# Optimization experiments

Measured on AMD Instinct MI355X. Metric: run time of the kernel, lower is better.

The kernel has to match this reference:

```python
import jax, jax.numpy as jnp
import numpy as np

TOP_K = 2
EPS = 1e-20


def setup_inputs() -> dict:
    key = jax.random.key(0)
    ks = jax.random.split(key, 8)
    B, S, H, E, D = 4, 2048, 1024, 8, 2048
    s = 0.02
    return {
        "x":  jax.random.normal(ks[0], (B, S, H), dtype=jnp.float32),
        "Wr": jax.random.normal(ks[1], (H, E), dtype=jnp.float32) * s,
        "Wg": jax.random.normal(ks[2], (E, H, D), dtype=jnp.float32) * s,
        "Wu": jax.random.normal(ks[3], (E, H, D), dtype=jnp.float32) * s,
        "Wd": jax.random.normal(ks[4], (E, D, H), dtype=jnp.float32) * s,
        "Sg": jax.random.normal(ks[5], (H, D), dtype=jnp.float32) * s,
        "Su": jax.random.normal(ks[6], (H, D), dtype=jnp.float32) * s,
        "Sd": jax.random.normal(ks[7], (D, H), dtype=jnp.float32) * s,
    }


def reference(x, Wr, Wg, Wu, Wd, Sg, Su, Sd):
    B, S, H = x.shape
    T = B * S
    xt = x.reshape(T, H)

    # Router: softmax scores, top-k, renormalize top-k weights
    scores = jax.nn.softmax(xt @ Wr, axis=-1)            # [T, E]
    topk_w, topk_idx = jax.lax.top_k(scores, TOP_K)      # [T, K]
    topk_w = topk_w / (topk_w.sum(axis=-1, keepdims=True) + EPS)

    # Per-expert SwiGLU FFN computed densely over all tokens (vectorized over E)
    g = jax.nn.silu(jnp.einsum('th,ehd->etd', xt, Wg))   # [E, T, D]
    u = jnp.einsum('th,ehd->etd', xt, Wu)                # [E, T, D]
    out_all = jnp.einsum('etd,edh->eth', g * u, Wd)      # [E, T, H]

    # Combine: gather each token's top-k expert outputs, weighted sum
    tok = jnp.arange(T)[:, None]                          # [T, 1]
    gathered = out_all[topk_idx, tok, :]                  # [T, K, H]
    out = jnp.sum(gathered * topk_w[..., None], axis=1).reshape(B, S, H)

    # Shared expert (applied to original input, added to MoE output)
    shared = (jax.nn.silu(x @ Sg) * (x @ Su)) @ Sd        # [B, S, H]
    return out + shared
```

## Files before the change

kernel.cpp:

```cpp
#include <hip/hip_runtime.h>
#include <stdint.h>

#define T_TOK 8192
#define HD 1024
#define ED 8
#define DD 2048
#define BM 128
#define BK 32
#define TILE_SHARED 64
#define TILE_MAX 200
#define ROWCAP 25600
#define RT_TPW 8

typedef short short8 __attribute__((ext_vector_type(8)));
typedef float f32x4 __attribute__((ext_vector_type(4)));

__device__ __forceinline__ unsigned short f2bf(float f) {
  union { float f; unsigned int u; } v; v.f = f;
  unsigned int r = (v.u + 0x7fffu + ((v.u >> 16) & 1u)) >> 16;
  return (unsigned short)r;
}

__device__ __forceinline__ void gll16(const void* g, void* l) {
  __builtin_amdgcn_global_load_lds(
      (const __attribute__((address_space(1))) unsigned int*)g,
      (__attribute__((address_space(3))) unsigned int*)l, 16, 0, 0);
}

__global__ __launch_bounds__(256) void k_zero(float* __restrict__ outp) {
  size_t i = (size_t)blockIdx.x * 256 + threadIdx.x;
  ((float4*)outp)[i] = make_float4(0.f, 0.f, 0.f, 0.f);
}

__global__ __launch_bounds__(256) void k_init(int* counts, int* tok, float* wrow) {
  int i = blockIdx.x * 256 + threadIdx.x;
  if (i < 32) counts[i] = 0;
  if (i < ROWCAP) {
    tok[i] = (i < T_TOK) ? i : 0;
    wrow[i] = (i < T_TOK) ? 1.0f : 0.0f;
  }
}

__global__ __launch_bounds__(256) void k_transpose(const float* __restrict__ in,
    unsigned short* __restrict__ outp, int R, int C) {
  __shared__ float tile[32][33];
  size_t boff = (size_t)blockIdx.z * (size_t)R * (size_t)C;
  in += boff; outp += boff;
  int c0 = blockIdx.x * 32, r0 = blockIdx.y * 32;
  int tx = threadIdx.x & 31, ty = threadIdx.x >> 5;
#pragma unroll
  for (int i = 0; i < 4; ++i)
    tile[ty + i * 8][tx] = in[(size_t)(r0 + ty + i * 8) * C + c0 + tx];
  __syncthreads();
#pragma unroll
  for (int i = 0; i < 4; ++i)
    outp[(size_t)(c0 + ty + i * 8) * R + r0 + tx] = f2bf(tile[tx][ty + i * 8]);
}

__global__ __launch_bounds__(256) void k_router(const float* __restrict__ x,
    const float* __restrict__ Wr, unsigned short* __restrict__ xb,
    int* __restrict__ counts, int* __restrict__ topE, float* __restrict__ topW) {
  __shared__ float wrT[ED * HD];
  __shared__ int hist[ED];
  int tid = threadIdx.x;
  if (tid < ED) hist[tid] = 0;
  for (int i = tid; i < ED * HD; i += 256) {
    int e = i >> 10, h = i & (HD - 1);
    wrT[i] = Wr[h * ED + e];
  }
  __syncthreads();
  int lane = tid & 63, wave = tid >> 6;
  int tbase = (blockIdx.x * 4 + wave) * RT_TPW;
  for (int tt = 0; tt < RT_TPW; ++tt) {
    int t = tbase + tt;
    const float* xrow = x + (size_t)t * HD;
    unsigned short* xbrow = xb + (size_t)t * HD;
    float acc[ED] = {0, 0, 0, 0, 0, 0, 0, 0};
#pragma unroll
    for (int i = 0; i < HD / 64; ++i) {
      int h = i * 64 + lane;
      float v = xrow[h];
      xbrow[h] = f2bf(v);
#pragma unroll
      for (int e = 0; e < ED; ++e) acc[e] += v * wrT[e * HD + h];
    }
#pragma unroll
    for (int off = 32; off; off >>= 1)
#pragma unroll
      for (int e = 0; e < ED; ++e) acc[e] += __shfl_xor(acc[e], off);
    if (lane == 0) {
      float m = acc[0];
#pragma unroll
      for (int e = 1; e < ED; ++e) m = fmaxf(m, acc[e]);
      float p[ED], s = 0.f;
#pragma unroll
      for (int e = 0; e < ED; ++e) { p[e] = __expf(acc[e] - m); s += p[e]; }
      int i0 = 0;
#pragma unroll
      for (int e = 1; e < ED; ++e) if (acc[e] > acc[i0]) i0 = e;
      int i1 = -1;
#pragma unroll
      for (int e = 0; e < ED; ++e) {
        if (e == i0) continue;
        if (i1 < 0 || acc[e] > acc[i1]) i1 = e;
      }
      float p0 = p[i0] / s, p1 = p[i1] / s;
      float rs = p0 + p1 + 1e-20f;
      topE[t * 2] = i0; topE[t * 2 + 1] = i1;
      topW[t * 2] = p0 / rs; topW[t * 2 + 1] = p1 / rs;
      atomicAdd(&hist[i0], 1);
      atomicAdd(&hist[i1], 1);
    }
  }
  __syncthreads();
  if (tid < ED) atomicAdd(&counts[tid], hist[tid]);
}

__global__ __launch_bounds__(256) void k_plan(const int* __restrict__ counts, int* cursor,
    int* __restrict__ tileE, int* __restrict__ tileEnd) {
  __shared__ int tstart[ED + 1], segend[ED];
  if (threadIdx.x == 0) {
    int base = T_TOK, rt = TILE_SHARED;
    for (int e = 0; e < ED; ++e) {
      int c = counts[e];
      cursor[e] = base;
      tstart[e] = rt;
      segend[e] = base + c;
      int tiles = (c + BM - 1) >> 7;
      rt += tiles;
      base += tiles << 7;
    }
    tstart[ED] = rt;
  }
  __syncthreads();
  for (int rt = threadIdx.x; rt < TILE_MAX; rt += 256) {
    int e = -1, end = 0;
    if (rt < TILE_SHARED) { e = ED; end = T_TOK; }
    else {
      for (int q = 0; q < ED; ++q)
        if (rt >= tstart[q] && rt < tstart[q + 1]) { e = q; end = segend[q]; }
    }
    tileE[rt] = e; tileEnd[rt] = end;
  }
}

__global__ __launch_bounds__(256) void k_scatter(const int* __restrict__ topE,
    const float* __restrict__ topW, int* cursor, int* tok, float* wrow) {
  __shared__ int lcount[ED], lbase[ED];
  int tid = threadIdx.x;
  if (tid < ED) lcount[tid] = 0;
  __syncthreads();
  int t = blockIdx.x * 256 + tid;
  int e0 = topE[t * 2], e1 = topE[t * 2 + 1];
  float w0 = topW[t * 2], w1 = topW[t * 2 + 1];
  int s0 = atomicAdd(&lcount[e0], 1);
  int s1 = atomicAdd(&lcount[e1], 1);
  __syncthreads();
  if (tid < ED) lbase[tid] = atomicAdd(&cursor[tid], lcount[tid]);
  __syncthreads();
  int p0 = lbase[e0] + s0;
  int p1 = lbase[e1] + s1;
  tok[p0] = t; wrow[p0] = w0;
  tok[p1] = t; wrow[p1] = w1;
}


__global__ __launch_bounds__(256, 2) void k_gemm1(
    const unsigned short* __restrict__ xb,
    const unsigned short* __restrict__ wgt, const unsigned short* __restrict__ wut,
    const unsigned short* __restrict__ sgt, const unsigned short* __restrict__ sut,
    const int* __restrict__ tok, const int* __restrict__ tileE,
    const int* __restrict__ tileEnd, unsigned short* __restrict__ hbuf, int tileBase) {
  int lt = blockIdx.y;
  int rt = tileBase + lt;
  int e = tileE[rt];
  if (e < 0) return;
  int n0 = blockIdx.x * BM;
  int grow0 = rt * BM;
  int hrow0 = lt * BM;
  int segEnd = tileEnd[rt];
  const unsigned short* bg = (e == ED) ? sgt : wgt + (size_t)e * DD * HD;
  const unsigned short* bu = (e == ED) ? sut : wut + (size_t)e * DD * HD;

  __shared__ __align__(16) unsigned short As[3][BM * BK];
  __shared__ __align__(16) unsigned short Bg[3][BM * BK];
  __shared__ __align__(16) unsigned short Bu[3][BM * BK];

  int tid = threadIdx.x, lane = tid & 63, wave = tid >> 6;
  int wm = (wave & 1) * 64, wn = (wave >> 1) * 64;
  int kc = (lane & 3) ^ ((lane >> 3) & 3);

  int ldsU[2];
  const unsigned short *pA[2], *pBg[2], *pBu[2];
#pragma unroll
  for (int r = 0; r < 2; ++r) {
    int chunk = r * 4 + wave;
    int row = chunk * 16 + (lane >> 2);
    ldsU[r] = chunk * 512;
    pA[r]  = xb + (size_t)tok[grow0 + row] * HD + kc * 8;
    pBg[r] = bg + (size_t)(n0 + row) * HD + kc * 8;
    pBu[r] = bu + (size_t)(n0 + row) * HD + kc * 8;
  }

  f32x4 zero = {0.f, 0.f, 0.f, 0.f};
  f32x4 accg[4][4], accu[4][4];
#pragma unroll
  for (int i = 0; i < 4; ++i)
#pragma unroll
    for (int j = 0; j < 4; ++j) { accg[i][j] = zero; accu[i][j] = zero; }

  int m15 = lane & 15;
  int sl8 = (((lane >> 4) ^ ((lane >> 1) & 3)) * 8);

#pragma unroll
  for (int r = 0; r < 2; ++r) {
    gll16(pA[r],  &As[0][ldsU[r]]);
    gll16(pBg[r], &Bg[0][ldsU[r]]);
    gll16(pBu[r], &Bu[0][ldsU[r]]);
  }
#pragma unroll
  for (int r = 0; r < 2; ++r) {
    gll16(pA[r] + BK,  &As[1][ldsU[r]]);
    gll16(pBg[r] + BK, &Bg[1][ldsU[r]]);
    gll16(pBu[r] + BK, &Bu[1][ldsU[r]]);
  }

  for (int k0 = 0; k0 < HD; k0 += BK) {
    int ti = k0 >> 5;
    int b  = ti % 3;
    if (k0 + BK < HD) asm volatile("s_waitcnt vmcnt(6)" ::: "memory");
    else              asm volatile("s_waitcnt vmcnt(0)" ::: "memory");
    __builtin_amdgcn_sched_barrier(0);
    __builtin_amdgcn_s_barrier();
    __builtin_amdgcn_sched_barrier(0);
    int k2 = k0 + 2 * BK;
    if (k2 < HD) {
      int b2 = (ti + 2) % 3;
#pragma unroll
      for (int r = 0; r < 2; ++r) {
        gll16(pA[r] + k2,  &As[b2][ldsU[r]]);
        gll16(pBg[r] + k2, &Bg[b2][ldsU[r]]);
        gll16(pBu[r] + k2, &Bu[b2][ldsU[r]]);
      }
    }
    __builtin_amdgcn_sched_barrier(0);
    short8 af[4], bgf[4], buf_[4];
#pragma unroll
    for (int i = 0; i < 4; ++i) {
      af[i]   = *(const short8*)(&As[b][(wm + i * 16 + m15) * BK + sl8]);
      bgf[i]  = *(const short8*)(&Bg[b][(wn + i * 16 + m15) * BK + sl8]);
      buf_[i] = *(const short8*)(&Bu[b][(wn + i * 16 + m15) * BK + sl8]);
    }
#pragma unroll
    for (int i = 0; i < 4; ++i)
#pragma unroll
      for (int j = 0; j < 4; ++j) {
        accg[i][j] = __builtin_amdgcn_mfma_f32_16x16x32_bf16(af[i], bgf[j],  accg[i][j], 0, 0, 0);
        accu[i][j] = __builtin_amdgcn_mfma_f32_16x16x32_bf16(af[i], buf_[j], accu[i][j], 0, 0, 0);
      }
    __builtin_amdgcn_sched_barrier(0);
  }

  int colB = n0 + wn + m15;
  int rowB = wm + ((lane >> 4) << 2);
#pragma unroll
  for (int i = 0; i < 4; ++i)
#pragma unroll
    for (int j = 0; j < 4; ++j)
#pragma unroll
      for (int r = 0; r < 4; ++r) {
        int lr = rowB + i * 16 + r;
        float g = accg[i][j][r], u = accu[i][j][r];
        float h = (grow0 + lr < segEnd) ? (g / (1.0f + __expf(-g))) * u : 0.0f;
        hbuf[(size_t)(hrow0 + lr) * DD + colB + j * 16] = f2bf(h);
      }
}

__global__ __launch_bounds__(256, 2) void k_gemm2(
    const unsigned short* __restrict__ hbuf,
    const unsigned short* __restrict__ wdt, const unsigned short* __restrict__ sdt,
    const int* __restrict__ tok, const int* __restrict__ tileE,
    const int* __restrict__ tileEnd, const float* __restrict__ wrow,
    float* __restrict__ outp, int tileBase) {
  int lt = blockIdx.y;
  int rt = tileBase + lt;
  int e = tileE[rt];
  if (e < 0) return;
  int n0 = blockIdx.x * BM;
  int grow0 = rt * BM;
  int hrow0 = lt * BM;
  int segEnd = tileEnd[rt];
  const unsigned short* bd = (e == ED) ? sdt : wdt + (size_t)e * HD * DD;

  __shared__ __align__(16) unsigned short As[3][BM * BK];
  __shared__ __align__(16) unsigned short Bs[3][BM * BK];

  int tid = threadIdx.x, lane = tid & 63, wave = tid >> 6;
  int wm = (wave & 1) * 64, wn = (wave >> 1) * 64;
  int kc = (lane & 3) ^ ((lane >> 3) & 3);

  int ldsU[2];
  const unsigned short *pA[2], *pB[2];
#pragma unroll
  for (int r = 0; r < 2; ++r) {
    int chunk = r * 4 + wave;
    int row = chunk * 16 + (lane >> 2);
    ldsU[r] = chunk * 512;
    pA[r] = hbuf + (size_t)(hrow0 + row) * DD + kc * 8;
    pB[r] = bd + (size_t)(n0 + row) * DD + kc * 8;
  }

  f32x4 zero = {0.f, 0.f, 0.f, 0.f};
  f32x4 acc[4][4];
#pragma unroll
  for (int i = 0; i < 4; ++i)
#pragma unroll
    for (int j = 0; j < 4; ++j) acc[i][j] = zero;

  int m15 = lane & 15;
  int sl8 = (((lane >> 4) ^ ((lane >> 1) & 3)) * 8);

#pragma unroll
  for (int r = 0; r < 2; ++r) {
    gll16(pA[r], &As[0][ldsU[r]]);
    gll16(pB[r], &Bs[0][ldsU[r]]);
  }
#pragma unroll
  for (int r = 0; r < 2; ++r) {
    gll16(pA[r] + BK, &As[1][ldsU[r]]);
    gll16(pB[r] + BK, &Bs[1][ldsU[r]]);
  }

  for (int k0 = 0; k0 < DD; k0 += BK) {
    int ti = k0 >> 5;
    int b  = ti % 3;
    if (k0 + BK < DD) asm volatile("s_waitcnt vmcnt(4)" ::: "memory");
    else              asm volatile("s_waitcnt vmcnt(0)" ::: "memory");
    __builtin_amdgcn_sched_barrier(0);
    __builtin_amdgcn_s_barrier();
    __builtin_amdgcn_sched_barrier(0);
    int k2 = k0 + 2 * BK;
    if (k2 < DD) {
      int b2 = (ti + 2) % 3;
#pragma unroll
      for (int r = 0; r < 2; ++r) {
        gll16(pA[r] + k2, &As[b2][ldsU[r]]);
        gll16(pB[r] + k2, &Bs[b2][ldsU[r]]);
      }
    }
    __builtin_amdgcn_sched_barrier(0);
    short8 af[4], bf[4];
#pragma unroll
    for (int i = 0; i < 4; ++i) {
      af[i] = *(const short8*)(&As[b][(wm + i * 16 + m15) * BK + sl8]);
      bf[i] = *(const short8*)(&Bs[b][(wn + i * 16 + m15) * BK + sl8]);
    }
#pragma unroll
    for (int i = 0; i < 4; ++i)
#pragma unroll
      for (int j = 0; j < 4; ++j)
        acc[i][j] = __builtin_amdgcn_mfma_f32_16x16x32_bf16(af[i], bf[j], acc[i][j], 0, 0, 0);
    __builtin_amdgcn_sched_barrier(0);
  }

  int colB = n0 + wn + m15;
  int rowB = wm + ((lane >> 4) << 2);
#pragma unroll
  for (int i = 0; i < 4; ++i)
#pragma unroll
    for (int r = 0; r < 4; ++r) {
      int grr = grow0 + rowB + i * 16 + r;
      if (grr < segEnd) {
        float w = wrow[grr];
        size_t ob = (size_t)tok[grr] * HD;
#pragma unroll
        for (int j = 0; j < 4; ++j)
          atomicAdd(&outp[ob + colB + j * 16], acc[i][j][r] * w);
      }
    }
}

extern "C" void kernel_launch(void* const* d_in, const int* in_sizes, int n_in,
                              void* d_out, int out_size, void* d_ws, size_t ws_size,
                              hipStream_t stream) {
  const float* x  = (const float*)d_in[0];
  const float* Wr = (const float*)d_in[1];
  const float* Wg = (const float*)d_in[2];
  const float* Wu = (const float*)d_in[3];
  const float* Wd = (const float*)d_in[4];
  const float* Sg = (const float*)d_in[5];
  const float* Su = (const float*)d_in[6];
  const float* Sd = (const float*)d_in[7];
  float* outp = (float*)d_out;

  size_t fixed = 0;
  auto pad = [](size_t b) { return (b + 255) & ~(size_t)255; };
  fixed += pad((size_t)T_TOK * HD * 2);
  fixed += pad((size_t)ED * DD * HD * 2) * 3;
  fixed += pad((size_t)DD * HD * 2) * 3;
  fixed += pad((size_t)ROWCAP * 4) * 2;
  fixed += pad((size_t)T_TOK * 2 * 4) * 2;
  fixed += pad(128) * 2 + pad(1024) * 2;
  int CH = TILE_MAX;
  if (fixed + pad((size_t)CH * BM * DD * 2) > ws_size) CH = TILE_MAX / 2;
  if (fixed + pad((size_t)CH * BM * DD * 2) > ws_size) return;

  char* ws = (char*)d_ws;
  size_t off = 0;
  auto alloc = [&](size_t bytes) -> char* {
    char* p = ws + off;
    off += (bytes + 255) & ~(size_t)255;
    return p;
  };
  unsigned short* xb  = (unsigned short*)alloc((size_t)T_TOK * HD * 2);
  unsigned short* wgt = (unsigned short*)alloc((size_t)ED * DD * HD * 2);
  unsigned short* wut = (unsigned short*)alloc((size_t)ED * DD * HD * 2);
  unsigned short* wdt = (unsigned short*)alloc((size_t)ED * HD * DD * 2);
  unsigned short* sgt = (unsigned short*)alloc((size_t)DD * HD * 2);
  unsigned short* sut = (unsigned short*)alloc((size_t)DD * HD * 2);
  unsigned short* sdt = (unsigned short*)alloc((size_t)HD * DD * 2);
  int* tok       = (int*)alloc((size_t)ROWCAP * 4);
  float* wrow    = (float*)alloc((size_t)ROWCAP * 4);
  int* topE      = (int*)alloc((size_t)T_TOK * 2 * 4);
  float* topW    = (float*)alloc((size_t)T_TOK * 2 * 4);
  int* counts    = (int*)alloc(128);
  int* cursor    = (int*)alloc(128);
  int* tileE     = (int*)alloc(1024);
  int* tileEnd   = (int*)alloc(1024);
  unsigned short* hbuf = (unsigned short*)alloc((size_t)CH * BM * DD * 2);

  k_zero<<<(out_size / 4 + 255) / 256, 256, 0, stream>>>(outp);
  k_init<<<(ROWCAP + 255) / 256, 256, 0, stream>>>(counts, tok, wrow);
  k_transpose<<<dim3(DD / 32, HD / 32, ED), 256, 0, stream>>>(Wg, wgt, HD, DD);
  k_transpose<<<dim3(DD / 32, HD / 32, ED), 256, 0, stream>>>(Wu, wut, HD, DD);
  k_transpose<<<dim3(HD / 32, DD / 32, ED), 256, 0, stream>>>(Wd, wdt, DD, HD);
  k_transpose<<<dim3(DD / 32, HD / 32, 1), 256, 0, stream>>>(Sg, sgt, HD, DD);
  k_transpose<<<dim3(DD / 32, HD / 32, 1), 256, 0, stream>>>(Su, sut, HD, DD);
  k_transpose<<<dim3(HD / 32, DD / 32, 1), 256, 0, stream>>>(Sd, sdt, DD, HD);
  k_router<<<T_TOK / (4 * RT_TPW), 256, 0, stream>>>(x, Wr, xb, counts, topE, topW);
  k_plan<<<1, 256, 0, stream>>>(counts, cursor, tileE, tileEnd);
  k_scatter<<<T_TOK / 256, 256, 0, stream>>>(topE, topW, cursor, tok, wrow);
  for (int cb = 0; cb < TILE_MAX; cb += CH) {
    k_gemm1<<<dim3(DD / BM, CH), 256, 0, stream>>>(xb, wgt, wut, sgt, sut, tok,
                                                   tileE, tileEnd, hbuf, cb);
    k_gemm2<<<dim3(HD / BM, CH), 256, 0, stream>>>(hbuf, wdt, sdt, tok, tileE,
                                                   tileEnd, wrow, outp, cb);
  }
}
```

Baseline: 812.0 us.

## Widen gate/up GEMM to 512-thread 128x256 tiles with split-phase ping-pong pipeline

The gate/up GEMM kernel now runs 8 waves per block over a 128x256 output tile, up from 4 waves over 128x128. Each K step splits into two phases: gate MFMAs, then up MFMAs. The global-to-LDS prefetch for the next stage is interleaved between the phases, with barriers and s_setprio raising priority around the MFMA bursts. The aim is to reuse the A tile across twice as many columns and overlap loads with math. The cost is more barriers per iteration and larger LDS use (about 120KB per block), which may limit residency to one block per CU.

```diff
diff --git a/kernel.cpp b/kernel.cpp
--- a/kernel.cpp
+++ b/kernel.cpp
@@ -165,7 +165,7 @@
 }
 
 
-__global__ __launch_bounds__(256, 2) void k_gemm1(
+__global__ __launch_bounds__(512, 2) void k_gemm1(
     const unsigned short* __restrict__ xb,
     const unsigned short* __restrict__ wgt, const unsigned short* __restrict__ wut,
     const unsigned short* __restrict__ sgt, const unsigned short* __restrict__ sut,
@@ -175,32 +175,29 @@
   int rt = tileBase + lt;
   int e = tileE[rt];
   if (e < 0) return;
-  int n0 = blockIdx.x * BM;
+  int n0 = blockIdx.x * 256;
   int grow0 = rt * BM;
   int hrow0 = lt * BM;
   int segEnd = tileEnd[rt];
   const unsigned short* bg = (e == ED) ? sgt : wgt + (size_t)e * DD * HD;
   const unsigned short* bu = (e == ED) ? sut : wut + (size_t)e * DD * HD;
 
-  __shared__ __align__(16) unsigned short As[3][BM * BK];
-  __shared__ __align__(16) unsigned short Bg[3][BM * BK];
-  __shared__ __align__(16) unsigned short Bu[3][BM * BK];
+  __shared__ __align__(16) unsigned short As3[3][4096];
+  __shared__ __align__(16) unsigned short Bg3[3][8192];
+  __shared__ __align__(16) unsigned short Bu3[3][8192];
 
   int tid = threadIdx.x, lane = tid & 63, wave = tid >> 6;
-  int wm = (wave & 1) * 64, wn = (wave >> 1) * 64;
+  int wm = (wave >> 2) * 64, wn = (wave & 3) * 64;
   int kc = (lane & 3) ^ ((lane >> 3) & 3);
-
-  int ldsU[2];
-  const unsigned short *pA[2], *pBg[2], *pBu[2];
-#pragma unroll
-  for (int r = 0; r < 2; ++r) {
-    int chunk = r * 4 + wave;
-    int row = chunk * 16 + (lane >> 2);
-    ldsU[r] = chunk * 512;
-    pA[r]  = xb + (size_t)tok[grow0 + row] * HD + kc * 8;
-    pBg[r] = bg + (size_t)(n0 + row) * HD + kc * 8;
-    pBu[r] = bu + (size_t)(n0 + row) * HD + kc * 8;
-  }
+  int rl = lane >> 2;
+
+  const unsigned short* pA  = xb + (size_t)tok[grow0 + wave * 16 + rl] * HD + kc * 8;
+  const unsigned short* pG0 = bg + (size_t)(n0 + wave * 32 + rl) * HD + kc * 8;
+  const unsigned short* pG1 = pG0 + (size_t)16 * HD;
+  const unsigned short* pU0 = bu + (size_t)(n0 + wave * 32 + rl) * HD + kc * 8;
+  const unsigned short* pU1 = pU0 + (size_t)16 * HD;
+  int dA = wave * 512;
+  int dB0 = wave * 1024, dB1 = wave * 1024 + 512;
 
   f32x4 zero = {0.f, 0.f, 0.f, 0.f};
   f32x4 accg[4][4], accu[4][4];
@@ -212,53 +209,83 @@
   int m15 = lane & 15;
   int sl8 = (((lane >> 4) ^ ((lane >> 1) & 3)) * 8);
 
-#pragma unroll
-  for (int r = 0; r < 2; ++r) {
-    gll16(pA[r],  &As[0][ldsU[r]]);
-    gll16(pBg[r], &Bg[0][ldsU[r]]);
-    gll16(pBu[r], &Bu[0][ldsU[r]]);
-  }
-#pragma unroll
-  for (int r = 0; r < 2; ++r) {
-    gll16(pA[r] + BK,  &As[1][ldsU[r]]);
-    gll16(pBg[r] + BK, &Bg[1][ldsU[r]]);
-    gll16(pBu[r] + BK, &Bu[1][ldsU[r]]);
-  }
-
-  for (int k0 = 0; k0 < HD; k0 += BK) {
-    int ti = k0 >> 5;
-    int b  = ti % 3;
-    if (k0 + BK < HD) asm volatile("s_waitcnt vmcnt(6)" ::: "memory");
-    else              asm volatile("s_waitcnt vmcnt(0)" ::: "memory");
+  gll16(pA,       &As3[0][dA]);
+  gll16(pG0,      &Bg3[0][dB0]);
+  gll16(pG1,      &Bg3[0][dB1]);
+  gll16(pU0,      &Bu3[0][dB0]);
+  gll16(pU1,      &Bu3[0][dB1]);
+  __builtin_amdgcn_sched_barrier(0);
+  gll16(pA + BK,  &As3[1][dA]);
+  gll16(pG0 + BK, &Bg3[1][dB0]);
+  gll16(pG1 + BK, &Bg3[1][dB1]);
+  gll16(pU0 + BK, &Bu3[1][dB0]);
+  gll16(pU1 + BK, &Bu3[1][dB1]);
+  __builtin_amdgcn_sched_barrier(0);
+  asm volatile("s_waitcnt vmcnt(5)" ::: "memory");
+  __builtin_amdgcn_sched_barrier(0);
+  __builtin_amdgcn_s_barrier();
+
+  int b = 0, bs = 2;
+  const int NT = HD / BK;
+  for (int t = 0; t < NT; ++t) {
+    bool pf = (t + 2 < NT);
+    int k2 = (t + 2) * BK;
+    const unsigned short* Ab = As3[b];
+    const unsigned short* Gb = Bg3[b];
+    const unsigned short* Ub = Bu3[b];
+
+    short8 af[4], bgf[4];
+#pragma unroll
+    for (int i = 0; i < 4; ++i) {
+      af[i]  = *(const short8*)(Ab + (wm + i * 16 + m15) * BK + sl8);
+      bgf[i] = *(const short8*)(Gb + (wn + i * 16 + m15) * BK + sl8);
+    }
+    if (pf) {
+      gll16(pA + k2,  &As3[bs][dA]);
+      gll16(pG0 + k2, &Bg3[bs][dB0]);
+      gll16(pG1 + k2, &Bg3[bs][dB1]);
+    }
     __builtin_amdgcn_sched_barrier(0);
     __builtin_amdgcn_s_barrier();
-    __builtin_amdgcn_sched_barrier(0);
-    int k2 = k0 + 2 * BK;
-    if (k2 < HD) {
-      int b2 = (ti + 2) % 3;
-#pragma unroll
-      for (int r = 0; r < 2; ++r) {
-        gll16(pA[r] + k2,  &As[b2][ldsU[r]]);
-        gll16(pBg[r] + k2, &Bg[b2][ldsU[r]]);
-        gll16(pBu[r] + k2, &Bu[b2][ldsU[r]]);
-      }
-    }
-    __builtin_amdgcn_sched_barrier(0);
-    short8 af[4], bgf[4], buf_[4];
-#pragma unroll
-    for (int i = 0; i < 4; ++i) {
-      af[i]   = *(const short8*)(&As[b][(wm + i * 16 + m15) * BK + sl8]);
-      bgf[i]  = *(const short8*)(&Bg[b][(wn + i * 16 + m15) * BK + sl8]);
-      buf_[i] = *(const short8*)(&Bu[b][(wn + i * 16 + m15) * BK + sl8]);
-    }
+    asm volatile("s_waitcnt lgkmcnt(0)" ::: "memory");
+    __builtin_amdgcn_sched_barrier(0);
+    __builtin_amdgcn_s_setprio(1);
 #pragma unroll
     for (int i = 0; i < 4; ++i)
 #pragma unroll
-      for (int j = 0; j < 4; ++j) {
-        accg[i][j] = __builtin_amdgcn_mfma_f32_16x16x32_bf16(af[i], bgf[j],  accg[i][j], 0, 0, 0);
+      for (int j = 0; j < 4; ++j)
+        accg[i][j] = __builtin_amdgcn_mfma_f32_16x16x32_bf16(af[i], bgf[j], accg[i][j], 0, 0, 0);
+    __builtin_amdgcn_s_setprio(0);
+    __builtin_amdgcn_sched_barrier(0);
+    __builtin_amdgcn_s_barrier();
+
+    short8 buf_[4];
+#pragma unroll
+    for (int j = 0; j < 4; ++j)
+      buf_[j] = *(const short8*)(Ub + (wn + j * 16 + m15) * BK + sl8);
+    if (pf) {
+      gll16(pU0 + k2, &Bu3[bs][dB0]);
+      gll16(pU1 + k2, &Bu3[bs][dB1]);
+    }
+    __builtin_amdgcn_sched_barrier(0);
+    if (pf) asm volatile("s_waitcnt vmcnt(5)" ::: "memory");
+    else    asm volatile("s_waitcnt vmcnt(0)" ::: "memory");
+    __builtin_amdgcn_sched_barrier(0);
+    __builtin_amdgcn_s_barrier();
+    asm volatile("s_waitcnt lgkmcnt(0)" ::: "memory");
+    __builtin_amdgcn_sched_barrier(0);
+    __builtin_amdgcn_s_setprio(1);
+#pragma unroll
+    for (int i = 0; i < 4; ++i)
+#pragma unroll
+      for (int j = 0; j < 4; ++j)
         accu[i][j] = __builtin_amdgcn_mfma_f32_16x16x32_bf16(af[i], buf_[j], accu[i][j], 0, 0, 0);
-      }
-    __builtin_amdgcn_sched_barrier(0);
+    __builtin_amdgcn_s_setprio(0);
+    __builtin_amdgcn_sched_barrier(0);
+    __builtin_amdgcn_s_barrier();
+
+    b = (b == 2) ? 0 : b + 1;
+    bs = (bs == 2) ? 0 : bs + 1;
   }
 
   int colB = n0 + wn + m15;
@@ -441,8 +468,8 @@
   k_plan<<<1, 256, 0, stream>>>(counts, cursor, tileE, tileEnd);
   k_scatter<<<T_TOK / 256, 256, 0, stream>>>(topE, topW, cursor, tok, wrow);
   for (int cb = 0; cb < TILE_MAX; cb += CH) {
-    k_gemm1<<<dim3(DD / BM, CH), 256, 0, stream>>>(xb, wgt, wut, sgt, sut, tok,
-                                                   tileE, tileEnd, hbuf, cb);
+    k_gemm1<<<dim3(DD / 256, CH), 512, 0, stream>>>(xb, wgt, wut, sgt, sut, tok,
+                                                    tileE, tileEnd, hbuf, cb);
     k_gemm2<<<dim3(HD / BM, CH), 256, 0, stream>>>(hbuf, wdt, sdt, tok, tileE,
                                                    tileEnd, wrow, outp, cb);
   }
```

Measured after the change: 816.0 us. Within noise of the previous version (+0.5%).
